# Performance work log

Measured on AMD Instinct MI355X. Metric: run time of the kernel, lower is better.

The kernel has to match this reference:

```python
import jax, jax.numpy as jnp
import numpy as np

NUM_LEVELS = 4
RADIUS = 4


def avg_pool2(x):
    # x: [N, H, W] -> [N, H//2, W//2] (kernel 2, stride 2 average pool)
    n, h, w = x.shape
    return x.reshape(n, h // 2, 2, w // 2, 2).mean(axis=(2, 4))


def bilinear_sample(img, x, y):
    # img: [N, H, W]; x, y: [N, S, S] absolute pixel coords (align_corners=True),
    # zero padding outside [0, W-1] x [0, H-1] (matches F.grid_sample defaults).
    n, h, w = img.shape
    x0 = jnp.floor(x)
    y0 = jnp.floor(y)
    wx1 = x - x0
    wy1 = y - y0
    wx0 = 1.0 - wx1
    wy0 = 1.0 - wy1
    nidx = jnp.arange(n)[:, None, None]

    def gather(yi, xi):
        valid = (xi >= 0) & (xi <= w - 1) & (yi >= 0) & (yi <= h - 1)
        xic = jnp.clip(xi, 0, w - 1).astype(jnp.int32)
        yic = jnp.clip(yi, 0, h - 1).astype(jnp.int32)
        return jnp.where(valid, img[nidx, yic, xic], 0.0)

    return (gather(y0, x0) * wy0 * wx0 + gather(y0, x0 + 1) * wy0 * wx1
            + gather(y0 + 1, x0) * wy1 * wx0 + gather(y0 + 1, x0 + 1) * wy1 * wx1)


def setup_inputs() -> dict:
    key = jax.random.key(0)
    k1, k2, k3 = jax.random.split(key, 3)
    b, c, h, w = 2, 256, 64, 64
    fmap1 = jax.random.normal(k1, (b, c, h, w), dtype=jnp.float32)
    fmap2 = jax.random.normal(k2, (b, c, h, w), dtype=jnp.float32)
    # absolute pixel (x, y) coordinates in [0, W-1] / [0, H-1]
    centroids_coords = jax.random.uniform(k3, (b, 2, h, w), dtype=jnp.float32) * (w - 1)
    return {"fmap1": fmap1, "fmap2": fmap2, "centroids_coords": centroids_coords}


def reference(fmap1, fmap2, centroids_coords):
    b, c, h1, w1 = fmap1.shape
    h2, w2 = fmap2.shape[-2:]
    # correlation volume: [b, h1*w1, h2*w2] / sqrt(c)
    f1 = fmap1.reshape(b, c, h1 * w1)
    f2 = fmap2.reshape(b, c, h2 * w2)
    corr = jnp.einsum('bcm,bcn->bmn', f1, f2) / jnp.sqrt(jnp.asarray(c, fmap1.dtype))
    corr = corr.reshape(b * h1 * w1, h2, w2)

    pyramid = [corr]
    for _ in range(NUM_LEVELS - 1):
        corr = avg_pool2(corr)
        pyramid.append(corr)

    side = 2 * RADIUS + 1
    di = jnp.linspace(-RADIUS, RADIUS, side)
    # delta[..., 0] = di (added to x), delta[..., 1] = dj (added to y) -- as in source
    delta = jnp.stack(jnp.meshgrid(di, di, indexing='ij'), axis=-1)  # [S, S, 2]

    cc = centroids_coords.transpose(0, 2, 3, 1).reshape(b * h1 * w1, 1, 1, 2)
    feats = []
    for lvl, vol in enumerate(pyramid):
        grid = cc / (2.0 ** lvl) + delta[None]  # [N, S, S, 2]
        sampled = bilinear_sample(vol, grid[..., 0], grid[..., 1])  # [N, S, S]
        feats.append(sampled.reshape(b, h1, w1, side * side))
    # [b, num_levels*side^2, h1, w1]
    return jnp.concatenate(feats, axis=-1).transpose(0, 3, 1, 2)
```

## Files before the change

### kernel.cpp

```cpp
#include <hip/hip_runtime.h>
#include <stdint.h>

#define M_DIM 4096
#define K_DIM 256

typedef unsigned short us;
typedef __attribute__((ext_vector_type(8))) short bf16x8;
typedef __attribute__((ext_vector_type(4))) float f32x4;

static __device__ __forceinline__ float bf2f(unsigned int u){
  unsigned int x = u << 16; float f;
  __builtin_memcpy(&f, &x, 4); return f;
}
static __device__ __forceinline__ us f2bf(float f){
  unsigned int x; __builtin_memcpy(&x, &f, 4);
  unsigned int r = x + 0x7fffu + ((x >> 16) & 1u);
  return (us)(r >> 16);
}
static __device__ __forceinline__ void gld16(const void* g, void* l){
  __builtin_amdgcn_global_load_lds(
      (const __attribute__((address_space(1))) unsigned int*)g,
      (__attribute__((address_space(3))) unsigned int*)l, 16, 0, 0);
}

__global__ void k_transpose_cast(const float* __restrict__ f1,
                                 const float* __restrict__ f2,
                                 us* __restrict__ A, us* __restrict__ B0){
  __shared__ float lds[64][65];
  int z = blockIdx.z;
  int b = z & 1, which = z >> 1;
  const float* in = which ? f2 : f1;
  us* out = which ? B0 : A;
  float scale = which ? 1.0f : 0.0625f;
  int c0 = blockIdx.y * 64, m0 = blockIdx.x * 64;
  const float* ib = in + (size_t)b * K_DIM * M_DIM;
  us* ob = out + (size_t)b * M_DIM * K_DIM;
  int t = threadIdx.x, r = t >> 6, j = t & 63;
#pragma unroll
  for (int k = 0; k < 16; k++)
    lds[r + k*4][j] = ib[(size_t)(c0 + r + k*4) * M_DIM + m0 + j];
  __syncthreads();
#pragma unroll
  for (int k = 0; k < 16; k++)
    ob[(size_t)(m0 + r + k*4) * K_DIM + c0 + j] = f2bf(lds[j][r + k*4] * scale);
}

__global__ void k_pool_all(const us* __restrict__ B0, us* __restrict__ B1,
                           us* __restrict__ B2, us* __restrict__ B3){
  int bid = blockIdx.x;
  us* dst; int wd, f;
  if (bid < 512)      { dst = B1; wd = 32; f = 2; }
  else if (bid < 640) { bid -= 512; dst = B2; wd = 16; f = 4; }
  else                { bid -= 640; dst = B3; wd = 8;  f = 8; }
  int t = threadIdx.x;
  int idx = bid * 4 + (t >> 6);
  int l = t & 63;
  int per = wd * wd;
  int b = idx / per, rem = idx - b * per;
  int y = rem / wd, x = rem - y * wd;
  const us* sb = B0 + (size_t)b * 4096 * K_DIM;
  float s0 = 0, s1 = 0, s2 = 0, s3 = 0;
  for (int dy = 0; dy < f; dy++)
    for (int dx = 0; dx < f; dx++){
      size_t off = ((size_t)(f*y + dy) * 64 + (f*x + dx)) * K_DIM + l * 4;
      uint2 v = *(const uint2*)(sb + off);
      s0 += bf2f(v.x & 0xffff); s1 += bf2f(v.x >> 16);
      s2 += bf2f(v.y & 0xffff); s3 += bf2f(v.y >> 16);
    }
  float inv = 1.0f / (float)(f * f);
  uint2 o;
  o.x = (unsigned)f2bf(s0*inv) | ((unsigned)f2bf(s1*inv) << 16);
  o.y = (unsigned)f2bf(s2*inv) | ((unsigned)f2bf(s3*inv) << 16);
  us* db = dst + (size_t)b * per * K_DIM;
  *(uint2*)(db + (size_t)rem * K_DIM + l * 4) = o;
}

__global__ __launch_bounds__(256) void k_gemm_all(
    const us* __restrict__ A,
    const us* __restrict__ B0, const us* __restrict__ B1,
    const us* __restrict__ B2, const us* __restrict__ B3,
    us* __restrict__ C0, us* __restrict__ C1,
    us* __restrict__ C2, us* __restrict__ C3){
  __shared__ __align__(16) us As[4096];
  __shared__ __align__(16) us Bs[4096];
  int bx = blockIdx.x;
  const us* B; us* C; int N, n0;
  if (bx < 32)      { B = B0; C = C0; N = 4096; n0 = bx * 128; }
  else if (bx < 40) { B = B1; C = C1; N = 1024; n0 = (bx - 32) * 128; }
  else if (bx < 42) { B = B2; C = C2; N = 256;  n0 = (bx - 40) * 128; }
  else              { B = B3; C = C3; N = 64;   n0 = 0; }
  int b = blockIdx.z;
  const us* Ab = A + (size_t)b * M_DIM * K_DIM;
  const us* Bb = B + (size_t)b * N * K_DIM;
  us* Cb = C + (size_t)b * M_DIM * N;
  int m0 = blockIdx.y * 128;
  int t = threadIdx.x;
  int wave = t >> 6, lane = t & 63;
  int wm = (wave >> 1) * 64, wn = (wave & 1) * 64;
  int srow = t >> 2, scol = (t & 3) * 8;
  int fr = lane & 15, fk = (lane >> 4) * 8;
  f32x4 acc[4][4];
#pragma unroll
  for (int i = 0; i < 4; i++)
#pragma unroll
    for (int j = 0; j < 4; j++) acc[i][j] = (f32x4){0.f, 0.f, 0.f, 0.f};

  int nr0 = n0 + srow;      if (nr0 > N - 1) nr0 = N - 1;
  int nr1 = n0 + srow + 64; if (nr1 > N - 1) nr1 = N - 1;
  const us* ga0 = Ab + (size_t)(m0 + srow) * K_DIM + scol;
  const us* ga1 = Ab + (size_t)(m0 + srow + 64) * K_DIM + scol;
  const us* gb0 = Bb + (size_t)nr0 * K_DIM + scol;
  const us* gb1 = Bb + (size_t)nr1 * K_DIM + scol;

  for (int kt = 0; kt < K_DIM; kt += 32){
    __syncthreads();
    gld16(ga0 + kt, As + t * 8);
    gld16(ga1 + kt, As + t * 8 + 2048);
    gld16(gb0 + kt, Bs + t * 8);
    gld16(gb1 + kt, Bs + t * 8 + 2048);
    asm volatile("s_waitcnt vmcnt(0)" ::: "memory");
    __syncthreads();
    bf16x8 af[4], bfv[4];
#pragma unroll
    for (int i = 0; i < 4; i++)
      af[i] = *(const bf16x8*)(As + (wm + i*16 + fr) * 32 + fk);
#pragma unroll
    for (int j = 0; j < 4; j++)
      bfv[j] = *(const bf16x8*)(Bs + (wn + j*16 + fr) * 32 + fk);
#pragma unroll
    for (int i = 0; i < 4; i++)
#pragma unroll
      for (int j = 0; j < 4; j++)
        acc[i][j] = __builtin_amdgcn_mfma_f32_16x16x32_bf16(af[i], bfv[j], acc[i][j], 0, 0, 0);
  }

  int cr = (lane >> 4) * 4, ccol = lane & 15;
#pragma unroll
  for (int i = 0; i < 4; i++){
#pragma unroll
    for (int j = 0; j < 4; j++){
      int col = n0 + wn + j*16 + ccol;
      if (col < N){
        size_t base = (size_t)(m0 + wm + i*16 + cr) * N + col;
#pragma unroll
        for (int r = 0; r < 4; r++)
          Cb[base + (size_t)r * N] = f2bf(acc[i][j][r]);
      }
    }
  }
}

__global__ __launch_bounds__(256) void k_sample(
    const us* __restrict__ p0, const us* __restrict__ p1,
    const us* __restrict__ p2, const us* __restrict__ p3,
    const float* __restrict__ cc, float* __restrict__ out){
  __shared__ float Wt[4][10][12];
  __shared__ float St[81][65];
  int i = blockIdx.x, b = blockIdx.y, lvl = blockIdx.z;
  int t = threadIdx.x, wv = t >> 6, lane = t & 63;
  const us* corr; int wl;
  if (lvl == 0)      { corr = p0; wl = 64; }
  else if (lvl == 1) { corr = p1; wl = 32; }
  else if (lvl == 2) { corr = p2; wl = 16; }
  else               { corr = p3; wl = 8;  }
  float inv = 1.0f / (float)(1 << lvl);
  int v = lane / 6, k = lane - v * 6;

  for (int rnd = 0; rnd < 16; rnd++){
    int jj = rnd * 4 + wv;
    int m = i * 64 + jj;
    const us* rowp = corr + (size_t)(b * M_DIM + m) * (wl * wl);
    float cx = cc[((size_t)(b*2 + 0) * 64 + i) * 64 + jj];
    float cy = cc[((size_t)(b*2 + 1) * 64 + i) * 64 + jj];
    float xs = cx * inv, ys = cy * inv;
    float x0f = floorf(xs), y0f = floorf(ys);
    int bx0 = (int)x0f - 4, by0 = (int)y0f - 4;
    float fx = xs - x0f, fy = ys - y0f;
    int e0 = bx0 & ~1, par = bx0 & 1;

    if (lane < 60){
      int ry = by0 + v;
      bool rok = (unsigned)ry < (unsigned)wl;
      int ryc = ry < 0 ? 0 : (ry > wl - 1 ? wl - 1 : ry);
      int si = e0 + 2 * k;
      int ec = si < 0 ? 0 : (si > wl - 2 ? wl - 2 : si);
      unsigned dv = *(const unsigned*)(rowp + ryc * wl + ec);
      float lo = (rok && (unsigned)si       < (unsigned)wl) ? bf2f(dv & 0xffff) : 0.0f;
      float hi = (rok && (unsigned)(si + 1) < (unsigned)wl) ? bf2f(dv >> 16)    : 0.0f;
      Wt[wv][v][2*k]     = lo;
      Wt[wv][v][2*k + 1] = hi;
    }
    float wx1 = fx, wx0 = 1.0f - fx, wy1 = fy, wy0 = 1.0f - fy;
#pragma unroll
    for (int p = 0; p < 2; p++){
      int o = lane + p * 64;
      if (o < 81){
        int a = o / 9, d = o - a * 9;
        float t00 = Wt[wv][d][a + par];
        float t01 = Wt[wv][d][a + par + 1];
        float t10 = Wt[wv][d + 1][a + par];
        float t11 = Wt[wv][d + 1][a + par + 1];
        St[o][jj] = wy0 * (wx0 * t00 + wx1 * t01) + wy1 * (wx0 * t10 + wx1 * t11);
      }
    }
  }

  __syncthreads();
  size_t ob = ((size_t)b * 324 + lvl * 81) * 4096 + (size_t)i * 64;
  int oo = t >> 6, j = t & 63;
#pragma unroll
  for (int r = 0; r < 21; r++){
    int o = oo + r * 4;
    if (o < 81)
      out[ob + (size_t)o * 4096 + j] = St[o][j];
  }
}

extern "C" void kernel_launch(void* const* d_in, const int* in_sizes, int n_in,
                              void* d_out, int out_size, void* d_ws, size_t ws_size,
                              hipStream_t stream){
  (void)in_sizes; (void)n_in; (void)out_size; (void)ws_size;
  const float* f1 = (const float*)d_in[0];
  const float* f2 = (const float*)d_in[1];
  const float* cc = (const float*)d_in[2];
  float* out = (float*)d_out;
  char* ws = (char*)d_ws;
  us* A  = (us*)(ws + 0);
  us* B0 = (us*)(ws + 4194304);
  us* B1 = (us*)(ws + 8388608);
  us* B2 = (us*)(ws + 9437184);
  us* B3 = (us*)(ws + 9699328);
  us* C0 = (us*)(ws + 9764864);
  us* C1 = (us*)(ws + 76873728);
  us* C2 = (us*)(ws + 93650944);
  us* C3 = (us*)(ws + 97845248);

  k_transpose_cast<<<dim3(64, 4, 4), dim3(256), 0, stream>>>(f1, f2, A, B0);
  k_pool_all<<<dim3(672), dim3(256), 0, stream>>>(B0, B1, B2, B3);
  k_gemm_all<<<dim3(43, 32, 2), dim3(256), 0, stream>>>(A, B0, B1, B2, B3, C0, C1, C2, C3);
  k_sample<<<dim3(64, 2, 4), dim3(256), 0, stream>>>(C0, C1, C2, C3, cc, out);
}
```

Measured before the change: 149.8 us.

## Fuse correlation GEMM with tap extraction, dropping full correlation volume writes

The GEMM epilogue now keeps only the 10x10 window of correlation values around each pixel's centroid and writes them into a compact fp32 taps buffer, instead of storing the whole bf16 correlation pyramid. A new combine kernel applies the bilinear weights from these taps. Each GEMM block also loops over several N tiles, which reduces grid size and reloads the A tile for every tile. This removes the large correlation-volume write and the scattered gather reads, at the cost of a memset, scattered epilogue stores, and fewer blocks, which lowers parallelism.

```diff
diff --git a/kernel.cpp b/kernel.cpp
--- a/kernel.cpp
+++ b/kernel.cpp
@@ -75,145 +75,135 @@
   *(uint2*)(db + (size_t)rem * K_DIM + l * 4) = o;
 }
 
-__global__ __launch_bounds__(256) void k_gemm_all(
+__global__ __launch_bounds__(256) void k_corr_taps(
     const us* __restrict__ A,
     const us* __restrict__ B0, const us* __restrict__ B1,
     const us* __restrict__ B2, const us* __restrict__ B3,
-    us* __restrict__ C0, us* __restrict__ C1,
-    us* __restrict__ C2, us* __restrict__ C3){
+    const float* __restrict__ cc, float* __restrict__ taps){
   __shared__ __align__(16) us As[4096];
   __shared__ __align__(16) us Bs[4096];
-  int bx = blockIdx.x;
-  const us* B; us* C; int N, n0;
-  if (bx < 32)      { B = B0; C = C0; N = 4096; n0 = bx * 128; }
-  else if (bx < 40) { B = B1; C = C1; N = 1024; n0 = (bx - 32) * 128; }
-  else if (bx < 42) { B = B2; C = C2; N = 256;  n0 = (bx - 40) * 128; }
-  else              { B = B3; C = C3; N = 64;   n0 = 0; }
-  int b = blockIdx.z;
+  __shared__ unsigned meta[128];
+  int bx = blockIdx.x, b = blockIdx.z, m0 = blockIdx.y * 128;
+  int lvl, ntiles, n0c;
+  const us* B;
+  if (bx < 8)       { lvl = 0; B = B0; ntiles = 4; n0c = bx * 512; }
+  else if (bx < 10) { lvl = 1; B = B1; ntiles = 4; n0c = (bx - 8) * 512; }
+  else if (bx == 10){ lvl = 2; B = B2; ntiles = 2; n0c = 0; }
+  else              { lvl = 3; B = B3; ntiles = 1; n0c = 0; }
+  int wl = 64 >> lvl, lsh = 6 - lvl, N = wl * wl;
+  float inv = 1.0f / (float)(1 << lvl);
+  int t = threadIdx.x;
+
+  if (t < 128){
+    int m = m0 + t;
+    float cx = cc[(size_t)b * 8192 + m];
+    float cy = cc[(size_t)b * 8192 + 4096 + m];
+    int px0 = (int)floorf(cx * inv) - 4;
+    int py0 = (int)floorf(cy * inv) - 4;
+    meta[t] = ((unsigned)(py0 + 8) << 16) | (unsigned)(px0 + 8);
+  }
+
   const us* Ab = A + (size_t)b * M_DIM * K_DIM;
   const us* Bb = B + (size_t)b * N * K_DIM;
-  us* Cb = C + (size_t)b * M_DIM * N;
-  int m0 = blockIdx.y * 128;
-  int t = threadIdx.x;
+  float* tb = taps + (size_t)(b * 4 + lvl) * 4096 * 128;
   int wave = t >> 6, lane = t & 63;
   int wm = (wave >> 1) * 64, wn = (wave & 1) * 64;
   int srow = t >> 2, scol = (t & 3) * 8;
   int fr = lane & 15, fk = (lane >> 4) * 8;
-  f32x4 acc[4][4];
-#pragma unroll
-  for (int i = 0; i < 4; i++)
-#pragma unroll
-    for (int j = 0; j < 4; j++) acc[i][j] = (f32x4){0.f, 0.f, 0.f, 0.f};
-
-  int nr0 = n0 + srow;      if (nr0 > N - 1) nr0 = N - 1;
-  int nr1 = n0 + srow + 64; if (nr1 > N - 1) nr1 = N - 1;
+  int cr = (lane >> 4) * 4, ccol = lane & 15;
   const us* ga0 = Ab + (size_t)(m0 + srow) * K_DIM + scol;
-  const us* ga1 = Ab + (size_t)(m0 + srow + 64) * K_DIM + scol;
-  const us* gb0 = Bb + (size_t)nr0 * K_DIM + scol;
-  const us* gb1 = Bb + (size_t)nr1 * K_DIM + scol;
-
-  for (int kt = 0; kt < K_DIM; kt += 32){
-    __syncthreads();
-    gld16(ga0 + kt, As + t * 8);
-    gld16(ga1 + kt, As + t * 8 + 2048);
-    gld16(gb0 + kt, Bs + t * 8);
-    gld16(gb1 + kt, Bs + t * 8 + 2048);
-    asm volatile("s_waitcnt vmcnt(0)" ::: "memory");
-    __syncthreads();
-    bf16x8 af[4], bfv[4];
+  const us* ga1 = ga0 + (size_t)64 * K_DIM;
+
+  for (int tile = 0; tile < ntiles; ++tile){
+    int n0 = n0c + tile * 128;
+    int nr0 = n0 + srow;      if (nr0 > N - 1) nr0 = N - 1;
+    int nr1 = n0 + srow + 64; if (nr1 > N - 1) nr1 = N - 1;
+    const us* gb0 = Bb + (size_t)nr0 * K_DIM + scol;
+    const us* gb1 = Bb + (size_t)nr1 * K_DIM + scol;
+
+    f32x4 acc[4][4];
 #pragma unroll
     for (int i = 0; i < 4; i++)
-      af[i] = *(const bf16x8*)(As + (wm + i*16 + fr) * 32 + fk);
-#pragma unroll
-    for (int j = 0; j < 4; j++)
-      bfv[j] = *(const bf16x8*)(Bs + (wn + j*16 + fr) * 32 + fk);
-#pragma unroll
-    for (int i = 0; i < 4; i++)
+#pragma unroll
+      for (int j = 0; j < 4; j++) acc[i][j] = (f32x4){0.f, 0.f, 0.f, 0.f};
+
+    for (int kt = 0; kt < K_DIM; kt += 32){
+      __syncthreads();
+      gld16(ga0 + kt, As + t * 8);
+      gld16(ga1 + kt, As + t * 8 + 2048);
+      gld16(gb0 + kt, Bs + t * 8);
+      gld16(gb1 + kt, Bs + t * 8 + 2048);
+      asm volatile("s_waitcnt vmcnt(0)" ::: "memory");
+      __syncthreads();
+      bf16x8 af[4], bfv[4];
+#pragma unroll
+      for (int i = 0; i < 4; i++)
+        af[i] = *(const bf16x8*)(As + (wm + i*16 + fr) * 32 + fk);
 #pragma unroll
       for (int j = 0; j < 4; j++)
-        acc[i][j] = __builtin_amdgcn_mfma_f32_16x16x32_bf16(af[i], bfv[j], acc[i][j], 0, 0, 0);
+        bfv[j] = *(const bf16x8*)(Bs + (wn + j*16 + fr) * 32 + fk);
+#pragma unroll
+      for (int i = 0; i < 4; i++)
+#pragma unroll
+        for (int j = 0; j < 4; j++)
+          acc[i][j] = __builtin_amdgcn_mfma_f32_16x16x32_bf16(af[i], bfv[j], acc[i][j], 0, 0, 0);
+    }
+
+#pragma unroll
+    for (int i = 0; i < 4; i++){
+#pragma unroll
+      for (int r = 0; r < 4; r++){
+        int lrow = wm + i*16 + cr + r;
+        unsigned mv = meta[lrow];
+        int px0 = (int)(mv & 0xffffu) - 8;
+        int py0 = (int)(mv >> 16) - 8;
+        float* pb = tb + (size_t)(m0 + lrow) * 128;
+#pragma unroll
+        for (int j = 0; j < 4; j++){
+          int col = n0 + wn + j*16 + ccol;
+          int y2 = col >> lsh, x2 = col & (wl - 1);
+          int dy = y2 - py0, dx = x2 - px0;
+          if ((unsigned)dy < 10u && (unsigned)dx < 10u && col < N)
+            pb[dy * 10 + dx] = acc[i][j][r];
+        }
+      }
+    }
   }
-
-  int cr = (lane >> 4) * 4, ccol = lane & 15;
-#pragma unroll
-  for (int i = 0; i < 4; i++){
-#pragma unroll
-    for (int j = 0; j < 4; j++){
-      int col = n0 + wn + j*16 + ccol;
-      if (col < N){
-        size_t base = (size_t)(m0 + wm + i*16 + cr) * N + col;
-#pragma unroll
-        for (int r = 0; r < 4; r++)
-          Cb[base + (size_t)r * N] = f2bf(acc[i][j][r]);
+}
+
+__global__ __launch_bounds__(256) void k_combine(
+    const float* __restrict__ taps, const float* __restrict__ cc,
+    float* __restrict__ out){
+  __shared__ float T[128 * 129];
+  int m0 = blockIdx.x * 128, b = blockIdx.y, lvl = blockIdx.z;
+  int t = threadIdx.x;
+  const float* src = taps + ((size_t)(b * 4 + lvl) * 4096 + m0) * 128;
+  for (int k = t; k < 16384; k += 256)
+    T[(k >> 7) * 129 + (k & 127)] = src[k];
+  __syncthreads();
+
+  int px = t & 127, half = t >> 7;
+  int m = m0 + px;
+  float inv = 1.0f / (float)(1 << lvl);
+  float cx = cc[(size_t)b * 8192 + m];
+  float cy = cc[(size_t)b * 8192 + 4096 + m];
+  float xs = cx * inv, ys = cy * inv;
+  float fx = xs - floorf(xs), fy = ys - floorf(ys);
+  float wx1 = fx, wx0 = 1.0f - fx, wy1 = fy, wy0 = 1.0f - fy;
+  const float* Tp = &T[px * 129];
+  size_t ob = ((size_t)b * 324 + lvl * 81) * 4096 + m;
+  int o_lo = half ? 41 : 0, o_hi = half ? 81 : 41;
+#pragma unroll
+  for (int a = 0; a < 9; a++)
+#pragma unroll
+    for (int d = 0; d < 9; d++){
+      int o = a * 9 + d;
+      if (o >= o_lo && o < o_hi){
+        float s = wy0 * (wx0 * Tp[d*10 + a]     + wx1 * Tp[d*10 + a + 1])
+                + wy1 * (wx0 * Tp[(d+1)*10 + a] + wx1 * Tp[(d+1)*10 + a + 1]);
+        out[ob + (size_t)o * 4096] = s;
       }
     }
-  }
-}
-
-__global__ __launch_bounds__(256) void k_sample(
-    const us* __restrict__ p0, const us* __restrict__ p1,
-    const us* __restrict__ p2, const us* __restrict__ p3,
-    const float* __restrict__ cc, float* __restrict__ out){
-  __shared__ float Wt[4][10][12];
-  __shared__ float St[81][65];
-  int i = blockIdx.x, b = blockIdx.y, lvl = blockIdx.z;
-  int t = threadIdx.x, wv = t >> 6, lane = t & 63;
-  const us* corr; int wl;
-  if (lvl == 0)      { corr = p0; wl = 64; }
-  else if (lvl == 1) { corr = p1; wl = 32; }
-  else if (lvl == 2) { corr = p2; wl = 16; }
-  else               { corr = p3; wl = 8;  }
-  float inv = 1.0f / (float)(1 << lvl);
-  int v = lane / 6, k = lane - v * 6;
-
-  for (int rnd = 0; rnd < 16; rnd++){
-    int jj = rnd * 4 + wv;
-    int m = i * 64 + jj;
-    const us* rowp = corr + (size_t)(b * M_DIM + m) * (wl * wl);
-    float cx = cc[((size_t)(b*2 + 0) * 64 + i) * 64 + jj];
-    float cy = cc[((size_t)(b*2 + 1) * 64 + i) * 64 + jj];
-    float xs = cx * inv, ys = cy * inv;
-    float x0f = floorf(xs), y0f = floorf(ys);
-    int bx0 = (int)x0f - 4, by0 = (int)y0f - 4;
-    float fx = xs - x0f, fy = ys - y0f;
-    int e0 = bx0 & ~1, par = bx0 & 1;
-
-    if (lane < 60){
-      int ry = by0 + v;
-      bool rok = (unsigned)ry < (unsigned)wl;
-      int ryc = ry < 0 ? 0 : (ry > wl - 1 ? wl - 1 : ry);
-      int si = e0 + 2 * k;
-      int ec = si < 0 ? 0 : (si > wl - 2 ? wl - 2 : si);
-      unsigned dv = *(const unsigned*)(rowp + ryc * wl + ec);
-      float lo = (rok && (unsigned)si       < (unsigned)wl) ? bf2f(dv & 0xffff) : 0.0f;
-      float hi = (rok && (unsigned)(si + 1) < (unsigned)wl) ? bf2f(dv >> 16)    : 0.0f;
-      Wt[wv][v][2*k]     = lo;
-      Wt[wv][v][2*k + 1] = hi;
-    }
-    float wx1 = fx, wx0 = 1.0f - fx, wy1 = fy, wy0 = 1.0f - fy;
-#pragma unroll
-    for (int p = 0; p < 2; p++){
-      int o = lane + p * 64;
-      if (o < 81){
-        int a = o / 9, d = o - a * 9;
-        float t00 = Wt[wv][d][a + par];
-        float t01 = Wt[wv][d][a + par + 1];
-        float t10 = Wt[wv][d + 1][a + par];
-        float t11 = Wt[wv][d + 1][a + par + 1];
-        St[o][jj] = wy0 * (wx0 * t00 + wx1 * t01) + wy1 * (wx0 * t10 + wx1 * t11);
-      }
-    }
-  }
-
-  __syncthreads();
-  size_t ob = ((size_t)b * 324 + lvl * 81) * 4096 + (size_t)i * 64;
-  int oo = t >> 6, j = t & 63;
-#pragma unroll
-  for (int r = 0; r < 21; r++){
-    int o = oo + r * 4;
-    if (o < 81)
-      out[ob + (size_t)o * 4096 + j] = St[o][j];
-  }
 }
 
 extern "C" void kernel_launch(void* const* d_in, const int* in_sizes, int n_in,
@@ -230,13 +220,11 @@
   us* B1 = (us*)(ws + 8388608);
   us* B2 = (us*)(ws + 9437184);
   us* B3 = (us*)(ws + 9699328);
-  us* C0 = (us*)(ws + 9764864);
-  us* C1 = (us*)(ws + 76873728);
-  us* C2 = (us*)(ws + 93650944);
-  us* C3 = (us*)(ws + 97845248);
+  float* taps = (float*)(ws + 9764864);
 
   k_transpose_cast<<<dim3(64, 4, 4), dim3(256), 0, stream>>>(f1, f2, A, B0);
   k_pool_all<<<dim3(672), dim3(256), 0, stream>>>(B0, B1, B2, B3);
-  k_gemm_all<<<dim3(43, 32, 2), dim3(256), 0, stream>>>(A, B0, B1, B2, B3, C0, C1, C2, C3);
-  k_sample<<<dim3(64, 2, 4), dim3(256), 0, stream>>>(C0, C1, C2, C3, cc, out);
-}
+  hipMemsetAsync(taps, 0, (size_t)2 * 4 * 4096 * 128 * 4, stream);
+  k_corr_taps<<<dim3(12, 32, 2), dim3(256), 0, stream>>>(A, B0, B1, B2, B3, cc, taps);
+  k_combine<<<dim3(32, 2, 4), dim3(256), 0, stream>>>(taps, cc, out);
+}
```

After: 164.4 us. +9.7%, slower.
